# Performance work log

Hardware: AMD Instinct MI355X
Metric: run time of the kernel (lower is better)

The kernel has to match this reference:

```python
import jax, jax.numpy as jnp
import numpy as np
import math

B, N = 64, 16384
POS_IN, HID, DIR_IN = 63, 128, 27
COLOR_IN = HID + DIR_IN  # 155
POS_W, POS_B = POS_IN * HID, HID          # 8064, 128
SIG_W, SIG_B = HID * 1, 1                  # 128, 1
COL_W, COL_B = COLOR_IN * 3, 3             # 465... actually 155*3=465? no: 465
TOTAL = POS_W + POS_B + SIG_W + SIG_B + COL_W + COL_B  # 8717


def pos_encode(x, num_freqs):
    # x: [..., 3] -> [..., 3 + 2*3*num_freqs], order: x, (sin f0, cos f0, sin f1, cos f1, ...)
    freqs = (2.0 ** jnp.arange(num_freqs, dtype=x.dtype)) * math.pi  # [L]
    xb = x[..., None, :] * freqs[:, None]                            # [..., L, 3]
    sc = jnp.stack([jnp.sin(xb), jnp.cos(xb)], axis=-2)              # [..., L, 2, 3]
    sc = sc.reshape(*x.shape[:-1], num_freqs * 2 * x.shape[-1])
    return jnp.concatenate([x, sc], axis=-1)


def setup_inputs() -> dict:
    key = jax.random.key(0)
    k1, k2, k3 = jax.random.split(key, 3)
    positions = jax.random.normal(k1, (B, N, 3), dtype=jnp.float32)
    directions = jax.random.normal(k2, (B, N, 3), dtype=jnp.float32)
    params = jax.random.normal(k3, (B, TOTAL), dtype=jnp.float32) * 0.1
    return {"positions": positions, "directions": directions, "params": params}


def reference(positions, directions, params):
    pos_enc = pos_encode(positions, 10)   # [B, N, 63]
    dir_enc = pos_encode(directions, 4)   # [B, N, 27]

    i = 0
    pw = params[:, i:i + POS_W].reshape(B, HID, POS_IN); i += POS_W
    pb = params[:, i:i + POS_B]; i += POS_B
    sw = params[:, i:i + SIG_W].reshape(B, 1, HID); i += SIG_W
    sb = params[:, i:i + SIG_B]; i += SIG_B
    cw = params[:, i:i + COL_W].reshape(B, 3, COLOR_IN); i += COL_W
    cb = params[:, i:i + COL_B]

    h = jnp.einsum('bnd,bhd->bnh', pos_enc, pw) + pb[:, None, :]
    h = jax.nn.relu(h)                                   # [B, N, 128]
    sigma = jnp.einsum('bnh,boh->bno', h, sw) + sb[:, None, :]  # [B, N, 1]
    h_dir = jnp.concatenate([h, dir_enc], axis=-1)       # [B, N, 155]
    rgb = jnp.einsum('bnc,boc->bno', h_dir, cw) + cb[:, None, :]
    rgb = jax.nn.sigmoid(rgb)                            # [B, N, 3]
    return sigma, rgb
```

## Files before the change

### kernel.cpp

```cpp
#include <hip/hip_runtime.h>
#include <hip/hip_bf16.h>


#define NB 64
#define NRAY 16384
#define NTOTAL 8789
#define NIT 8

typedef short bf16x8 __attribute__((ext_vector_type(8)));
typedef float f32x16 __attribute__((ext_vector_type(16)));

union U8 { unsigned u[4]; bf16x8 v; };

__device__ __forceinline__ unsigned pk2(float a, float b) {
    float2 t; t.x = a; t.y = b;
    __hip_bfloat162 h = __float22bfloat162_rn(t);
    return *reinterpret_cast<unsigned*>(&h);
}

#define MFMA __builtin_amdgcn_mfma_f32_32x32x16_bf16

__global__ __launch_bounds__(256, 2) void nerf_mfma_kernel(
    const float* __restrict__ pos,
    const float* __restrict__ dir,
    const float* __restrict__ params,
    float* __restrict__ out)
{
    const int tid  = threadIdx.x;
    const int lane = tid & 63;
    const int wid  = tid >> 6;
    const int hi   = lane >> 5;
    const int l31  = lane & 31;

    const int b     = blockIdx.x >> 3;
    const int chunk = (blockIdx.x & 7) << 11;
    const float* __restrict__ p = params + b * NTOTAL;

    __shared__ uint4 encs[2048];
    __shared__ unsigned hawLds[256];
    char* encb = reinterpret_cast<char*>(encs);
    const char* hawb = reinterpret_cast<const char*>(hawLds);

    if (tid < 64) {
        const int s  = tid & 7;
        const int hh = (tid >> 3) & 1;
        const int r  = tid >> 4;
        const float* w2 = (r == 0) ? (p + 8192) : (p + 8321 + (r - 1) * 155);
        const int base = 32 * (s >> 1) + 16 * (s & 1) + 4 * hh;
        unsigned* dst = &hawLds[(((s << 1) + hh) * 4 + r) * 4];
        #pragma unroll
        for (int j = 0; j < 4; ++j) {
            const int i0 = 2 * j, i1 = 2 * j + 1;
            dst[j] = pk2(w2[base + (i0 & 3) + 8 * (i0 >> 2)],
                         w2[base + (i1 & 3) + 8 * (i1 >> 2)]);
        }
    }

    bf16x8 aw[4][4];
    #pragma unroll
    for (int mt = 0; mt < 4; ++mt) {
        const int hrow = mt * 32 + l31;
        const float* wrow = p + hrow * 63;
        const float bias = p[8064 + hrow];
        #pragma unroll
        for (int ks = 0; ks < 4; ++ks) {
            U8 u;
            #pragma unroll
            for (int j = 0; j < 4; ++j) {
                const int k0 = ks * 16 + hi * 8 + 2 * j;
                const int k1 = k0 + 1;
                const float e0 = (k0 < 3) ? wrow[k0] : (k0 == 3 ? bias : wrow[k0 - 1]);
                const float e1 = (k1 < 3) ? wrow[k1] : (k1 == 3 ? bias : wrow[k1 - 1]);
                u.u[j] = pk2(e0, e1);
            }
            aw[mt][ks] = u.v;
        }
    }

    f32x16 FZ;
    #pragma unroll
    for (int i = 0; i < 16; ++i) FZ[i] = 0.f;

    const float sb  = p[8320];
    const float cb0 = p[8786], cb1 = p[8787], cb2 = p[8788];
    const float* __restrict__ cwr  = p + 8321 + 128;
    const float* __restrict__ cwg  = p + 8321 + 155 + 128;
    const float* __restrict__ cwb2 = p + 8321 + 310 + 128;

    const int rayBlock = b * NRAY + chunk;
    float* __restrict__ rgbout = out + (long)NB * NRAY;
    const long pb0 = (long)(rayBlock + tid) * 3;
    const int hoff = hi * 64 + (l31 & 3) * 16;

    auto encode_row = [&](const float3 Pv) {
        const int swz = (tid & 7) << 4;
        char* myrow = encb + tid * 128;
        float s0 = __builtin_amdgcn_sinf(0.5f * Pv.x), c0 = __builtin_amdgcn_cosf(0.5f * Pv.x);
        float s1 = __builtin_amdgcn_sinf(0.5f * Pv.y), c1 = __builtin_amdgcn_cosf(0.5f * Pv.y);
        float s2 = __builtin_amdgcn_sinf(0.5f * Pv.z), c2 = __builtin_amdgcn_cosf(0.5f * Pv.z);
        unsigned wb[4];
        wb[0] = pk2(Pv.x, Pv.y);
        wb[1] = pk2(Pv.z, 1.0f);
        #pragma unroll
        for (int f = 0; f < 10; ++f) {
            const int w = 2 + 3 * f;
            wb[(w + 0) & 3] = pk2(s0, s1);
            if (((w + 0) & 3) == 3) {
                uint4 v; v.x = wb[0]; v.y = wb[1]; v.z = wb[2]; v.w = wb[3];
                *reinterpret_cast<uint4*>(myrow + ((((w + 0) >> 2) * 16) ^ swz)) = v;
            }
            wb[(w + 1) & 3] = pk2(s2, c0);
            if (((w + 1) & 3) == 3) {
                uint4 v; v.x = wb[0]; v.y = wb[1]; v.z = wb[2]; v.w = wb[3];
                *reinterpret_cast<uint4*>(myrow + ((((w + 1) >> 2) * 16) ^ swz)) = v;
            }
            wb[(w + 2) & 3] = pk2(c1, c2);
            if (((w + 2) & 3) == 3) {
                uint4 v; v.x = wb[0]; v.y = wb[1]; v.z = wb[2]; v.w = wb[3];
                *reinterpret_cast<uint4*>(myrow + ((((w + 2) >> 2) * 16) ^ swz)) = v;
            }
            if (f < 9) {
                float t;
                t = 2.f * s0 * c0; c0 = fmaf(-2.f * s0, s0, 1.f); s0 = t;
                t = 2.f * s1 * c1; c1 = fmaf(-2.f * s1, s1, 1.f); s1 = t;
                t = 2.f * s2 * c2; c2 = fmaf(-2.f * s2, s2, 1.f); s2 = t;
            }
        }
    };

    float3 Pc = *reinterpret_cast<const float3*>(pos + pb0);
    float3 Pn = *reinterpret_cast<const float3*>(pos + pb0 + 768);
    float3 Dc = *reinterpret_cast<const float3*>(dir + pb0);
    float3 Dn = *reinterpret_cast<const float3*>(dir + pb0 + 768);
    encode_row(Pc);
    __syncthreads();

    #pragma unroll 1
    for (int it = 0; it < NIT; ++it) {
        const int ray = rayBlock + it * 256 + tid;

        float3 Pn2, Dn2;
        if (it < NIT - 2) {
            Pn2 = *reinterpret_cast<const float3*>(pos + pb0 + (it + 2) * 768);
            Dn2 = *reinterpret_cast<const float3*>(dir + pb0 + (it + 2) * 768);
        }

        bf16x8 be0[4], be1[4];
        {
            const int row0 = wid * 64 + l31;
            const int swz0 = (row0 & 7) << 4;
            const int row1 = row0 + 32;
            const int swz1 = (row1 & 7) << 4;
            #pragma unroll
            for (int ks = 0; ks < 4; ++ks) {
                be0[ks] = *reinterpret_cast<const bf16x8*>(
                    encb + row0 * 128 + ((ks * 32 + hi * 16) ^ swz0));
                be1[ks] = *reinterpret_cast<const bf16x8*>(
                    encb + row1 * 128 + ((ks * 32 + hi * 16) ^ swz1));
            }
        }

        if (it < NIT - 1) encode_row(Pn);

        float crd = 0.f, cgd = 0.f, cbd = 0.f;
        {
            float s0 = __builtin_amdgcn_sinf(0.5f * Dc.x), c0 = __builtin_amdgcn_cosf(0.5f * Dc.x);
            float s1 = __builtin_amdgcn_sinf(0.5f * Dc.y), c1 = __builtin_amdgcn_cosf(0.5f * Dc.y);
            float s2 = __builtin_amdgcn_sinf(0.5f * Dc.z), c2 = __builtin_amdgcn_cosf(0.5f * Dc.z);
            crd = fmaf(Dc.x, cwr[0], crd);  cgd = fmaf(Dc.x, cwg[0], cgd);  cbd = fmaf(Dc.x, cwb2[0], cbd);
            crd = fmaf(Dc.y, cwr[1], crd);  cgd = fmaf(Dc.y, cwg[1], cgd);  cbd = fmaf(Dc.y, cwb2[1], cbd);
            crd = fmaf(Dc.z, cwr[2], crd);  cgd = fmaf(Dc.z, cwg[2], cgd);  cbd = fmaf(Dc.z, cwb2[2], cbd);
            #pragma unroll
            for (int f = 0; f < 4; ++f) {
                const int j = 3 + 6 * f;
                crd = fmaf(s0, cwr[j+0], crd); cgd = fmaf(s0, cwg[j+0], cgd); cbd = fmaf(s0, cwb2[j+0], cbd);
                crd = fmaf(s1, cwr[j+1], crd); cgd = fmaf(s1, cwg[j+1], cgd); cbd = fmaf(s1, cwb2[j+1], cbd);
                crd = fmaf(s2, cwr[j+2], crd); cgd = fmaf(s2, cwg[j+2], cgd); cbd = fmaf(s2, cwb2[j+2], cbd);
                crd = fmaf(c0, cwr[j+3], crd); cgd = fmaf(c0, cwg[j+3], cgd); cbd = fmaf(c0, cwb2[j+3], cbd);
                crd = fmaf(c1, cwr[j+4], crd); cgd = fmaf(c1, cwg[j+4], cgd); cbd = fmaf(c1, cwb2[j+4], cbd);
                crd = fmaf(c2, cwr[j+5], crd); cgd = fmaf(c2, cwg[j+5], cgd); cbd = fmaf(c2, cwb2[j+5], cbd);
                if (f < 3) {
                    float t;
                    t = 2.f * s0 * c0; c0 = fmaf(-2.f * s0, s0, 1.f); s0 = t;
                    t = 2.f * s1 * c1; c1 = fmaf(-2.f * s1, s1, 1.f); s1 = t;
                    t = 2.f * s2 * c2; c2 = fmaf(-2.f * s2, s2, 1.f); s2 = t;
                }
            }
        }

        __builtin_amdgcn_s_setprio(1);
        f32x16 hacc0, hacc1;
        #pragma unroll
        for (int mt = 0; mt < 4; ++mt) {
            f32x16 a0 = MFMA(aw[mt][0], be0[0], FZ, 0, 0, 0);
            f32x16 a1 = MFMA(aw[mt][0], be1[0], FZ, 0, 0, 0);
            a0 = MFMA(aw[mt][1], be0[1], a0, 0, 0, 0);
            a1 = MFMA(aw[mt][1], be1[1], a1, 0, 0, 0);
            a0 = MFMA(aw[mt][2], be0[2], a0, 0, 0, 0);
            a1 = MFMA(aw[mt][2], be1[2], a1, 0, 0, 0);
            a0 = MFMA(aw[mt][3], be0[3], a0, 0, 0, 0);
            a1 = MFMA(aw[mt][3], be1[3], a1, 0, 0, 0);

            #pragma unroll
            for (int t = 0; t < 2; ++t) {
                const int rb = t * 8;
                const int s = 2 * mt + t;
                U8 u0, u1;
                #pragma unroll
                for (int j = 0; j < 4; ++j) {
                    u0.u[j] = pk2(fmaxf(a0[rb + 2 * j], 0.f),
                                  fmaxf(a0[rb + 2 * j + 1], 0.f));
                    u1.u[j] = pk2(fmaxf(a1[rb + 2 * j], 0.f),
                                  fmaxf(a1[rb + 2 * j + 1], 0.f));
                }
                const bf16x8 hw = *reinterpret_cast<const bf16x8*>(
                    hawb + s * 128 + hoff);
                hacc0 = MFMA(hw, u0.v, (s == 0) ? FZ : hacc0, 0, 0, 0);
                hacc1 = MFMA(hw, u1.v, (s == 0) ? FZ : hacc1, 0, 0, 0);
            }
        }
        __builtin_amdgcn_s_setprio(0);

        const float hv0 = hi ? hacc1[0] : hacc0[0];
        const float hv1 = hi ? hacc1[1] : hacc0[1];
        const float hv2 = hi ? hacc1[2] : hacc0[2];
        const float hv3 = hi ? hacc1[3] : hacc0[3];

        const float sig = hv0 + sb;
        float cr  = hv1 + cb0 + crd;
        float cg  = hv2 + cb1 + cgd;
        float cbl = hv3 + cb2 + cbd;

        cr  = 1.0f / (1.0f + __expf(-cr));
        cg  = 1.0f / (1.0f + __expf(-cg));
        cbl = 1.0f / (1.0f + __expf(-cbl));

        out[ray] = sig;
        float3 rgbv; rgbv.x = cr; rgbv.y = cg; rgbv.z = cbl;
        *reinterpret_cast<float3*>(rgbout + (long)ray * 3) = rgbv;

        Pn = Pn2; Dc = Dn; Dn = Dn2;
    }
}

extern "C" void kernel_launch(void* const* d_in, const int* in_sizes, int n_in,
                              void* d_out, int out_size, void* d_ws, size_t ws_size,
                              hipStream_t stream) {
    const float* pos    = (const float*)d_in[0];
    const float* dirs   = (const float*)d_in[1];
    const float* params = (const float*)d_in[2];
    float* out = (float*)d_out;

    dim3 grid(512);
    dim3 block(256);
    nerf_mfma_kernel<<<grid, block, 0, stream>>>(pos, dirs, params, out);
}
```

Before: 47.59 us.

## Move direction encoding and color-head dot products onto MFMA via LDS

Replaces the per-thread scalar FMA evaluation of the direction-encoding contribution to sigma/RGB (81 FMAs plus biases per ray) with two extra MFMA steps. Direction encodings are packed into bf16 rows in a new swizzled LDS buffer, and biases are folded in through a constant-1 column. The aim is to cut VALU work and the scalar parameter loads. In exchange it adds LDS footprint and writes, extra LDS reads, and bf16 rounding of the direction terms and biases.

New measurement: 51.26 us. 7.7% more time.

```diff
diff --git a/kernel.cpp b/kernel.cpp
--- a/kernel.cpp
+++ b/kernel.cpp
@@ -37,8 +37,10 @@
     const float* __restrict__ p = params + b * NTOTAL;
 
     __shared__ uint4 encs[2048];
-    __shared__ unsigned hawLds[256];
+    __shared__ uint4 dirs[1024];
+    __shared__ unsigned hawLds[320];
     char* encb = reinterpret_cast<char*>(encs);
+    char* dirb = reinterpret_cast<char*>(dirs);
     const char* hawb = reinterpret_cast<const char*>(hawLds);
 
     if (tid < 64) {
@@ -54,6 +56,22 @@
             dst[j] = pk2(w2[base + (i0 & 3) + 8 * (i0 >> 2)],
                          w2[base + (i1 & 3) + 8 * (i1 >> 2)]);
         }
+    } else if (tid < 80) {
+        const int t2 = tid - 64;
+        const int s  = 8 + (t2 & 1);
+        const int hh = (t2 >> 1) & 1;
+        const int r  = t2 >> 2;
+        const float* w2 = (r == 0) ? (p + 8192) : (p + 8321 + (r - 1) * 155);
+        const float bias2 = (r == 0) ? p[8320] : p[8786 + r - 1];
+        unsigned* dst = &hawLds[(((s << 1) + hh) * 4 + r) * 4];
+        #pragma unroll
+        for (int j = 0; j < 4; ++j) {
+            const int d0 = (s - 8) * 16 + hh * 8 + 2 * j;
+            const int d1 = d0 + 1;
+            const float e0 = (d0 == 27) ? bias2 : ((d0 < 27 && r > 0) ? w2[128 + d0] : 0.f);
+            const float e1 = (d1 == 27) ? bias2 : ((d1 < 27 && r > 0) ? w2[128 + d1] : 0.f);
+            dst[j] = pk2(e0, e1);
+        }
     }
 
     bf16x8 aw[4][4];
@@ -80,12 +98,6 @@
     f32x16 FZ;
     #pragma unroll
     for (int i = 0; i < 16; ++i) FZ[i] = 0.f;
-
-    const float sb  = p[8320];
-    const float cb0 = p[8786], cb1 = p[8787], cb2 = p[8788];
-    const float* __restrict__ cwr  = p + 8321 + 128;
-    const float* __restrict__ cwg  = p + 8321 + 155 + 128;
-    const float* __restrict__ cwb2 = p + 8321 + 310 + 128;
 
     const int rayBlock = b * NRAY + chunk;
     float* __restrict__ rgbout = out + (long)NB * NRAY;
@@ -128,11 +140,48 @@
         }
     };
 
+    auto encode_dir = [&](const float3 Dv) {
+        const int row  = tid >> 1;
+        const int half = tid & 1;
+        const int dswz = (row & 7) << 4;
+        char* base = dirb + row * 128;
+        float s0 = __builtin_amdgcn_sinf(0.5f * Dv.x), c0 = __builtin_amdgcn_cosf(0.5f * Dv.x);
+        float s1 = __builtin_amdgcn_sinf(0.5f * Dv.y), c1 = __builtin_amdgcn_cosf(0.5f * Dv.y);
+        float s2 = __builtin_amdgcn_sinf(0.5f * Dv.z), c2 = __builtin_amdgcn_cosf(0.5f * Dv.z);
+        unsigned wd[16];
+        wd[0] = pk2(Dv.x, Dv.y);
+        wd[1] = pk2(Dv.z, s0);
+        wd[2] = pk2(s1, s2);
+        wd[3] = pk2(c0, c1);
+        #pragma unroll
+        for (int f = 1; f < 4; ++f) {
+            const float c2p = c2;
+            float t;
+            t = 2.f * s0 * c0; c0 = fmaf(-2.f * s0, s0, 1.f); s0 = t;
+            t = 2.f * s1 * c1; c1 = fmaf(-2.f * s1, s1, 1.f); s1 = t;
+            t = 2.f * s2 * c2; c2 = fmaf(-2.f * s2, s2, 1.f); s2 = t;
+            wd[1 + 3 * f] = pk2(c2p, s0);
+            wd[2 + 3 * f] = pk2(s1, s2);
+            wd[3 + 3 * f] = pk2(c0, c1);
+        }
+        wd[13] = pk2(c2, 1.0f);
+        wd[14] = 0u;
+        wd[15] = 0u;
+        #pragma unroll
+        for (int c = 0; c < 4; ++c) {
+            uint4 v;
+            v.x = wd[4 * c + 0]; v.y = wd[4 * c + 1];
+            v.z = wd[4 * c + 2]; v.w = wd[4 * c + 3];
+            *reinterpret_cast<uint4*>(base + ((half * 64 + c * 16) ^ dswz)) = v;
+        }
+    };
+
     float3 Pc = *reinterpret_cast<const float3*>(pos + pb0);
     float3 Pn = *reinterpret_cast<const float3*>(pos + pb0 + 768);
     float3 Dc = *reinterpret_cast<const float3*>(dir + pb0);
     float3 Dn = *reinterpret_cast<const float3*>(dir + pb0 + 768);
     encode_row(Pc);
+    encode_dir(Dc);
     __syncthreads();
 
     #pragma unroll 1
@@ -145,7 +194,7 @@
             Dn2 = *reinterpret_cast<const float3*>(dir + pb0 + (it + 2) * 768);
         }
 
-        bf16x8 be0[4], be1[4];
+        bf16x8 be0[4], be1[4], bd0[2], bd1[2];
         {
             const int row0 = wid * 64 + l31;
             const int swz0 = (row0 & 7) << 4;
@@ -158,38 +207,32 @@
                 be1[ks] = *reinterpret_cast<const bf16x8*>(
                     encb + row1 * 128 + ((ks * 32 + hi * 16) ^ swz1));
             }
-        }
-
-        if (it < NIT - 1) encode_row(Pn);
-
-        float crd = 0.f, cgd = 0.f, cbd = 0.f;
-        {
-            float s0 = __builtin_amdgcn_sinf(0.5f * Dc.x), c0 = __builtin_amdgcn_cosf(0.5f * Dc.x);
-            float s1 = __builtin_amdgcn_sinf(0.5f * Dc.y), c1 = __builtin_amdgcn_cosf(0.5f * Dc.y);
-            float s2 = __builtin_amdgcn_sinf(0.5f * Dc.z), c2 = __builtin_amdgcn_cosf(0.5f * Dc.z);
-            crd = fmaf(Dc.x, cwr[0], crd);  cgd = fmaf(Dc.x, cwg[0], cgd);  cbd = fmaf(Dc.x, cwb2[0], cbd);
-            crd = fmaf(Dc.y, cwr[1], crd);  cgd = fmaf(Dc.y, cwg[1], cgd);  cbd = fmaf(Dc.y, cwb2[1], cbd);
-            crd = fmaf(Dc.z, cwr[2], crd);  cgd = fmaf(Dc.z, cwg[2], cgd);  cbd = fmaf(Dc.z, cwb2[2], cbd);
-            #pragma unroll
-            for (int f = 0; f < 4; ++f) {
-                const int j = 3 + 6 * f;
-                crd = fmaf(s0, cwr[j+0], crd); cgd = fmaf(s0, cwg[j+0], cgd); cbd = fmaf(s0, cwb2[j+0], cbd);
-                crd = fmaf(s1, cwr[j+1], crd); cgd = fmaf(s1, cwg[j+1], cgd); cbd = fmaf(s1, cwb2[j+1], cbd);
-                crd = fmaf(s2, cwr[j+2], crd); cgd = fmaf(s2, cwg[j+2], cgd); cbd = fmaf(s2, cwb2[j+2], cbd);
-                crd = fmaf(c0, cwr[j+3], crd); cgd = fmaf(c0, cwg[j+3], cgd); cbd = fmaf(c0, cwb2[j+3], cbd);
-                crd = fmaf(c1, cwr[j+4], crd); cgd = fmaf(c1, cwg[j+4], cgd); cbd = fmaf(c1, cwb2[j+4], cbd);
-                crd = fmaf(c2, cwr[j+5], crd); cgd = fmaf(c2, cwg[j+5], cgd); cbd = fmaf(c2, cwb2[j+5], cbd);
-                if (f < 3) {
-                    float t;
-                    t = 2.f * s0 * c0; c0 = fmaf(-2.f * s0, s0, 1.f); s0 = t;
-                    t = 2.f * s1 * c1; c1 = fmaf(-2.f * s1, s1, 1.f); s1 = t;
-                    t = 2.f * s2 * c2; c2 = fmaf(-2.f * s2, s2, 1.f); s2 = t;
-                }
-            }
+            const int dr0 = row0 >> 1, dh0 = row0 & 1, dsz0 = (dr0 & 7) << 4;
+            const int dr1 = row1 >> 1, dh1 = row1 & 1, dsz1 = (dr1 & 7) << 4;
+            #pragma unroll
+            for (int t = 0; t < 2; ++t) {
+                bd0[t] = *reinterpret_cast<const bf16x8*>(
+                    dirb + dr0 * 128 + ((dh0 * 64 + t * 32 + hi * 16) ^ dsz0));
+                bd1[t] = *reinterpret_cast<const bf16x8*>(
+                    dirb + dr1 * 128 + ((dh1 * 64 + t * 32 + hi * 16) ^ dsz1));
+            }
+        }
+
+        if (it < NIT - 1) {
+            encode_dir(Dn);
+            encode_row(Pn);
         }
 
         __builtin_amdgcn_s_setprio(1);
         f32x16 hacc0, hacc1;
+        {
+            const bf16x8 hw8 = *reinterpret_cast<const bf16x8*>(hawb + 8 * 128 + hoff);
+            const bf16x8 hw9 = *reinterpret_cast<const bf16x8*>(hawb + 9 * 128 + hoff);
+            hacc0 = MFMA(hw8, bd0[0], FZ, 0, 0, 0);
+            hacc1 = MFMA(hw8, bd1[0], FZ, 0, 0, 0);
+            hacc0 = MFMA(hw9, bd0[1], hacc0, 0, 0, 0);
+            hacc1 = MFMA(hw9, bd1[1], hacc1, 0, 0, 0);
+        }
         #pragma unroll
         for (int mt = 0; mt < 4; ++mt) {
             f32x16 a0 = MFMA(aw[mt][0], be0[0], FZ, 0, 0, 0);
@@ -215,21 +258,16 @@
                 }
                 const bf16x8 hw = *reinterpret_cast<const bf16x8*>(
                     hawb + s * 128 + hoff);
-                hacc0 = MFMA(hw, u0.v, (s == 0) ? FZ : hacc0, 0, 0, 0);
-                hacc1 = MFMA(hw, u1.v, (s == 0) ? FZ : hacc1, 0, 0, 0);
+                hacc0 = MFMA(hw, u0.v, hacc0, 0, 0, 0);
+                hacc1 = MFMA(hw, u1.v, hacc1, 0, 0, 0);
             }
         }
         __builtin_amdgcn_s_setprio(0);
 
-        const float hv0 = hi ? hacc1[0] : hacc0[0];
-        const float hv1 = hi ? hacc1[1] : hacc0[1];
-        const float hv2 = hi ? hacc1[2] : hacc0[2];
-        const float hv3 = hi ? hacc1[3] : hacc0[3];
-
-        const float sig = hv0 + sb;
-        float cr  = hv1 + cb0 + crd;
-        float cg  = hv2 + cb1 + cgd;
-        float cbl = hv3 + cb2 + cbd;
+        const float sig = hi ? hacc1[0] : hacc0[0];
+        float cr  = hi ? hacc1[1] : hacc0[1];
+        float cg  = hi ? hacc1[2] : hacc0[2];
+        float cbl = hi ? hacc1[3] : hacc0[3];
 
         cr  = 1.0f / (1.0f + __expf(-cr));
         cg  = 1.0f / (1.0f + __expf(-cg));
```
